# Kernel tuning notes

Hardware: AMD Instinct MI355X
Metric: run time of the kernel (lower is better)

Reference implementation:

```python
import jax, jax.numpy as jnp
import numpy as np

B, S, D, H = 2, 2048, 512, 8


def setup_inputs() -> dict:
    key = jax.random.key(0)
    ks = jax.random.split(key, 9)
    scale = 1.0 / np.sqrt(D)
    x = jax.random.normal(ks[0], (B, S, D), dtype=jnp.float32)
    # Per-head full-width projections, stacked over heads: [H, D, D]
    Wq = jax.random.normal(ks[1], (H, D, D), dtype=jnp.float32) * scale
    Wk = jax.random.normal(ks[2], (H, D, D), dtype=jnp.float32) * scale
    Wv = jax.random.normal(ks[3], (H, D, D), dtype=jnp.float32) * scale
    bq = jax.random.normal(ks[4], (H, D), dtype=jnp.float32) * 0.01
    bk = jax.random.normal(ks[5], (H, D), dtype=jnp.float32) * 0.01
    bv = jax.random.normal(ks[6], (H, D), dtype=jnp.float32) * 0.01
    Wo = jax.random.normal(ks[7], (H * D, D), dtype=jnp.float32) * (1.0 / np.sqrt(H * D))
    bo = jax.random.normal(ks[8], (D,), dtype=jnp.float32) * 0.01
    return {"x": x, "Wq": Wq, "bq": bq, "Wk": Wk, "bk": bk, "Wv": Wv, "bv": bv, "Wo": Wo, "bo": bo}


def reference(x, Wq, bq, Wk, bk, Wv, bv, Wo, bo):
    # Batched per-head projections: [B,S,D] x [H,D,E] -> [B,H,S,E]
    q = jnp.einsum('bsd,hde->bhse', x, Wq) + bq[None, :, None, :]
    k = jnp.einsum('bsd,hde->bhse', x, Wk) + bk[None, :, None, :]
    v = jnp.einsum('bsd,hde->bhse', x, Wv) + bv[None, :, None, :]
    # NOTE: original module has NO 1/sqrt(d) scaling
    scores = jnp.einsum('bhse,bhte->bhst', q, k)  # [B,H,S,S]
    attn = jax.nn.softmax(scores, axis=-1)
    out = jnp.einsum('bhst,bhte->bhse', attn, v)  # [B,H,S,D]
    # Concat heads along feature dim: [B,S,H*D]
    cat = out.transpose(0, 2, 1, 3).reshape(B, S, H * D)
    return cat @ Wo + bo
```

## Files before the change

### kernel.cpp

```cpp
#include <hip/hip_runtime.h>

typedef _Float16 f16;
typedef _Float16 f16x8 __attribute__((ext_vector_type(8)));
typedef float f32x4 __attribute__((ext_vector_type(4)));

#define B_ 2
#define S_ 2048
#define D_ 512
#define H_ 8

__device__ inline void async_ld16(const void* g, void* l) {
  __builtin_amdgcn_global_load_lds((__attribute__((address_space(1))) void*)(g),
                                   (__attribute__((address_space(3))) void*)(l),
                                   16, 0, 0);
}

__global__ __launch_bounds__(256) void cvt_f16(const float* __restrict__ src,
                                               f16* __restrict__ dst, long n) {
  long i = (long)blockIdx.x * 256 + threadIdx.x;
  if (i >= n) return;
  dst[i] = (f16)src[i];
}

__global__ __launch_bounds__(256) void transpose_f32(const float* __restrict__ src,
                                                     f16* __restrict__ dst, int R, int C) {
  __shared__ float t[32][33];
  size_t zoff = (size_t)blockIdx.z * R * C;
  const float* s = src + zoff;
  int tx = threadIdx.x;
  int ty = threadIdx.y;
  int c0 = blockIdx.x * 32, r0 = blockIdx.y * 32;
#pragma unroll
  for (int i = 0; i < 4; ++i)
    t[ty + i * 8][tx] = s[(size_t)(r0 + ty + i * 8) * C + c0 + tx];
  __syncthreads();
#pragma unroll
  for (int i = 0; i < 4; ++i)
    dst[zoff + (size_t)(c0 + ty + i * 8) * R + r0 + tx] = (f16)t[tx][ty + i * 8];
}

__global__ __launch_bounds__(256) void reduce_out(const float* __restrict__ part,
                                                  const float* __restrict__ bo,
                                                  float* __restrict__ out, long n, int nslab) {
  long i = (long)blockIdx.x * 256 + threadIdx.x;
  if (i >= n) return;
  float v = bo[i & (D_ - 1)];
  for (int s = 0; s < nslab; ++s) v += part[(long)s * n + i];
  out[i] = v;
}

struct GemmArgs {
  const f16 *A, *Bm;
  void* C;
  const float* bias;
  float* Mloc;
  int K, lda, ldb, ldc;
  int zbase, NG, PBG;
  long sAp, sAb, sAg, sAz;
  long sBp, sBb, sBg, sBz;
  long sCp, sCb, sCg, sCz;
  long sbp, sbb, sbg, sbz;
  long sMlz;
};

template <typename OutT, int BIAS, bool PEXP>
__global__ __launch_bounds__(256) void gemm_nt(GemmArgs p) {
  int zloc = blockIdx.z;
  int zi = p.zbase + zloc;
  int pp = zi / p.PBG; int rz = zi - pp * p.PBG;
  int bb = rz / p.NG;  int g = rz - bb * p.NG;
  const f16* A  = p.A + (pp * p.sAp + bb * p.sAb + g * p.sAg + (long)zloc * p.sAz);
  const f16* Bm = p.Bm + (pp * p.sBp + bb * p.sBb + g * p.sBg + (long)zloc * p.sBz);
  OutT* C = (OutT*)p.C + (pp * p.sCp + bb * p.sCb + g * p.sCg + (long)zloc * p.sCz);
  const float* bias = nullptr;
  if (BIAS) bias = p.bias + (pp * p.sbp + bb * p.sbb + g * p.sbg + (long)zloc * p.sbz);

  __shared__ f16 lA[4096];
  __shared__ f16 lB[4096];
  __shared__ float lMx[PEXP ? 256 : 1];

  int tid = threadIdx.x;
  int lane = tid & 63;
  int w = tid >> 6;
  int wm = (w >> 1) << 6;
  int wn = (w & 1) << 6;
  long bm = (long)blockIdx.y * 128;
  long bn = (long)blockIdx.x * 128;

  f32x4 acc[4][4] = {};
  int qd = lane >> 4;
  int fr = lane & 15;

  int q0 = tid, q1 = tid + 256;
  int r0s = q0 >> 2, c0s = (q0 & 3) ^ ((r0s >> 1) & 3);
  int r1s = q1 >> 2, c1s = (q1 & 3) ^ ((r1s >> 1) & 3);

  for (int k0 = 0; k0 < p.K; k0 += 32) {
    long oa0 = (bm + r0s) * (long)p.lda + (k0 + c0s * 8);
    long oa1 = (bm + r1s) * (long)p.lda + (k0 + c1s * 8);
    long ob0 = (bn + r0s) * (long)p.ldb + (k0 + c0s * 8);
    long ob1 = (bn + r1s) * (long)p.ldb + (k0 + c1s * 8);
    __syncthreads();
    async_ld16(A + oa0,  lA + (size_t)q0 * 8);
    async_ld16(A + oa1,  lA + (size_t)q1 * 8);
    async_ld16(Bm + ob0, lB + (size_t)q0 * 8);
    async_ld16(Bm + ob1, lB + (size_t)q1 * 8);
    __syncthreads();

    f16x8 ah[4], bh[4];
#pragma unroll
    for (int i = 0; i < 4; ++i) {
      int m = wm + i * 16 + fr;
      ah[i] = *(const f16x8*)(lA + ((size_t)m * 4 + (qd ^ ((m >> 1) & 3))) * 8);
      int n = wn + i * 16 + fr;
      bh[i] = *(const f16x8*)(lB + ((size_t)n * 4 + (qd ^ ((n >> 1) & 3))) * 8);
    }
#pragma unroll
    for (int i = 0; i < 4; ++i)
#pragma unroll
      for (int j = 0; j < 4; ++j)
        acc[i][j] = __builtin_amdgcn_mfma_f32_16x16x32_f16(ah[i], bh[j], acc[i][j], 0, 0, 0);
  }

  int rr0 = qd * 4;
  if (PEXP) {
#pragma unroll
    for (int i = 0; i < 4; ++i) {
#pragma unroll
      for (int r = 0; r < 4; ++r) {
        float v = fmaxf(fmaxf(acc[i][0][r], acc[i][1][r]),
                        fmaxf(acc[i][2][r], acc[i][3][r]));
        v = fmaxf(v, __shfl_xor(v, 1, 64));
        v = fmaxf(v, __shfl_xor(v, 2, 64));
        v = fmaxf(v, __shfl_xor(v, 4, 64));
        v = fmaxf(v, __shfl_xor(v, 8, 64));
        if (fr == 0) lMx[(w & 1) * 128 + wm + i * 16 + rr0 + r] = v;
      }
    }
    __syncthreads();
    if (tid < 128) {
      float ml = fmaxf(lMx[tid], lMx[128 + tid]);
      p.Mloc[(long)zloc * p.sMlz + (long)blockIdx.x * S_ + bm + tid] = ml;
    }
#pragma unroll
    for (int i = 0; i < 4; ++i) {
#pragma unroll
      for (int r = 0; r < 4; ++r) {
        int rl = wm + i * 16 + rr0 + r;
        float ml = fmaxf(lMx[rl], lMx[128 + rl]);
        long row = bm + rl;
#pragma unroll
        for (int j = 0; j < 4; ++j) {
          long col = bn + wn + j * 16 + fr;
          ((f16*)C)[row * (long)p.ldc + col] = (f16)__expf(acc[i][j][r] - ml);
        }
      }
    }
  } else {
#pragma unroll
    for (int i = 0; i < 4; ++i) {
#pragma unroll
      for (int j = 0; j < 4; ++j) {
#pragma unroll
        for (int r = 0; r < 4; ++r) {
          long row = bm + wm + i * 16 + rr0 + r;
          long col = bn + wn + j * 16 + fr;
          float v = acc[i][j][r];
          if (BIAS == 1) v += bias[col];
          if (BIAS == 2) v += bias[row];
          C[row * (long)p.ldc + col] = (OutT)v;
        }
      }
    }
  }
}

struct QkvArgs {
  const f16 *xh, *wqk, *wv;
  f16 *qk, *vT;
  const float *bqk, *bv;
};
__global__ __launch_bounds__(256) void qkv_proj(QkvArgs p) {
  const long SD = (long)S_ * D_, DD = (long)D_ * D_, DS = (long)D_ * S_;
  int zi = blockIdx.z;
  int pp = zi >> 4;
  int r = zi & 15;
  int b = r >> 3, h = r & 7;
  int bid = blockIdx.x;
  const f16 *A, *Bm;
  f16* C;
  const float* bias;
  long bm, bn;
  int ldc;
  bool biasRow;
  if (pp < 2) {
    A = p.xh + (long)b * SD;
    Bm = p.wqk + ((long)pp * 8 + h) * DD;
    C = p.qk + (long)zi * SD;
    bias = p.bqk + ((long)pp * 8 + h) * D_;
    bm = (long)(bid >> 2) * 128; bn = (long)(bid & 3) * 128;
    ldc = D_; biasRow = false;
  } else {
    A = p.wv + (long)h * DD;
    Bm = p.xh + (long)b * SD;
    C = p.vT + (long)(b * 8 + h) * DS;
    bias = p.bv + (long)h * D_;
    bm = (long)(bid >> 4) * 128; bn = (long)(bid & 15) * 128;
    ldc = S_; biasRow = true;
  }

  __shared__ f16 lA[4096];
  __shared__ f16 lB[4096];

  int tid = threadIdx.x;
  int lane = tid & 63;
  int w = tid >> 6;
  int wm = (w >> 1) << 6;
  int wn = (w & 1) << 6;

  f32x4 acc[4][4] = {};
  int qd = lane >> 4;
  int fr = lane & 15;

  int q0 = tid, q1 = tid + 256;
  int r0s = q0 >> 2, c0s = (q0 & 3) ^ ((r0s >> 1) & 3);
  int r1s = q1 >> 2, c1s = (q1 & 3) ^ ((r1s >> 1) & 3);

  for (int k0 = 0; k0 < D_; k0 += 32) {
    long oa0 = (bm + r0s) * (long)D_ + (k0 + c0s * 8);
    long oa1 = (bm + r1s) * (long)D_ + (k0 + c1s * 8);
    long ob0 = (bn + r0s) * (long)D_ + (k0 + c0s * 8);
    long ob1 = (bn + r1s) * (long)D_ + (k0 + c1s * 8);
    __syncthreads();
    async_ld16(A + oa0,  lA + (size_t)q0 * 8);
    async_ld16(A + oa1,  lA + (size_t)q1 * 8);
    async_ld16(Bm + ob0, lB + (size_t)q0 * 8);
    async_ld16(Bm + ob1, lB + (size_t)q1 * 8);
    __syncthreads();

    f16x8 ah[4], bh[4];
#pragma unroll
    for (int i = 0; i < 4; ++i) {
      int m = wm + i * 16 + fr;
      ah[i] = *(const f16x8*)(lA + ((size_t)m * 4 + (qd ^ ((m >> 1) & 3))) * 8);
      int n = wn + i * 16 + fr;
      bh[i] = *(const f16x8*)(lB + ((size_t)n * 4 + (qd ^ ((n >> 1) & 3))) * 8);
    }
#pragma unroll
    for (int i = 0; i < 4; ++i)
#pragma unroll
      for (int j = 0; j < 4; ++j)
        acc[i][j] = __builtin_amdgcn_mfma_f32_16x16x32_f16(ah[i], bh[j], acc[i][j], 0, 0, 0);
  }

  int rr0 = qd * 4;
#pragma unroll
  for (int i = 0; i < 4; ++i) {
#pragma unroll
    for (int j = 0; j < 4; ++j) {
#pragma unroll
      for (int r = 0; r < 4; ++r) {
        long row = bm + wm + i * 16 + rr0 + r;
        long col = bn + wn + j * 16 + fr;
        float v = acc[i][j][r] + (biasRow ? bias[row] : bias[col]);
        C[row * (long)ldc + col] = (f16)v;
      }
    }
  }
}

struct PvArgs {
  const f16* S; const float* Ml; const f16* V; f16* C;
  int ldc, zbase, NG;
  long sVz, sCb, sCg;
};
__global__ __launch_bounds__(256) void pv_flash(PvArgs p) {
  int zloc = blockIdx.z;
  int zi = p.zbase + zloc;
  int bb = zi / p.NG; int g = zi - bb * p.NG;
  const f16* Sm = p.S + (long)zloc * S_ * S_;
  const float* Ml = p.Ml + (long)zloc * 16 * S_;
  const f16* V = p.V + (long)zloc * p.sVz;
  f16* C = p.C + bb * p.sCb + g * p.sCg;

  __shared__ f16 lP[2][64 * 32];
  __shared__ f16 lV[2][128 * 32];

  int tid = threadIdx.x;
  int lane = tid & 63;
  int w = tid >> 6;
  long bm = (long)blockIdx.y * 64;
  long bn = (long)blockIdx.x * 128;
  int e0 = (w & 1) << 6;
  int m0 = (w >> 1) << 5;

  int qd = lane >> 4;
  int fr = lane & 15;

  f32x4 acc[2][4] = {};
  f32x4 lacc[2] = {};
  f16x8 ones;
#pragma unroll
  for (int j = 0; j < 8; ++j) ones[j] = (f16)1.0f;

  float mg[2];
#pragma unroll
  for (int i = 0; i < 2; ++i) {
    float m = -1e30f;
#pragma unroll
    for (int cb = 0; cb < 16; ++cb)
      m = fmaxf(m, Ml[cb * S_ + bm + m0 + i * 16 + fr]);
    mg[i] = m;
  }
  f16 al16[2];

  int rs = tid >> 2, cs = (tid & 3) ^ ((rs >> 1) & 3);

  for (int k0 = 0; k0 < S_; k0 += 64) {
    if ((k0 & 127) == 0) {
      int cb = k0 >> 7;
#pragma unroll
      for (int i = 0; i < 2; ++i)
        al16[i] = (f16)__expf(Ml[cb * S_ + bm + m0 + i * 16 + fr] - mg[i]);
    }
    __syncthreads();
#pragma unroll
    for (int t = 0; t < 2; ++t) {
      async_ld16(Sm + (bm + rs) * (long)S_ + (k0 + t * 32 + cs * 8),
                 lP[t] + (size_t)tid * 8);
#pragma unroll
      for (int j = 0; j < 2; ++j) {
        int q = j * 256 + tid;
        int rv = q >> 2, cv = (q & 3) ^ ((rv >> 1) & 3);
        async_ld16(V + (bn + rv) * (long)S_ + (k0 + t * 32 + cv * 8),
                   lV[t] + (size_t)q * 8);
      }
    }
    __syncthreads();

#pragma unroll
    for (int t = 0; t < 2; ++t) {
      f16x8 ah[2], bh[4];
#pragma unroll
      for (int i = 0; i < 2; ++i) {
        int m = m0 + i * 16 + fr;
        ah[i] = *(const f16x8*)(lP[t] + ((size_t)m * 4 + (qd ^ ((m >> 1) & 3))) * 8);
#pragma unroll
        for (int j = 0; j < 8; ++j) ah[i][j] *= al16[i];
      }
#pragma unroll
      for (int j = 0; j < 4; ++j) {
        int n = e0 + j * 16 + fr;
        bh[j] = *(const f16x8*)(lV[t] + ((size_t)n * 4 + (qd ^ ((n >> 1) & 3))) * 8);
      }
#pragma unroll
      for (int i = 0; i < 2; ++i) {
        lacc[i] = __builtin_amdgcn_mfma_f32_16x16x32_f16(ah[i], ones, lacc[i], 0, 0, 0);
#pragma unroll
        for (int j = 0; j < 4; ++j)
          acc[i][j] = __builtin_amdgcn_mfma_f32_16x16x32_f16(ah[i], bh[j], acc[i][j], 0, 0, 0);
      }
    }
  }

  int rr0 = qd * 4;
#pragma unroll
  for (int i = 0; i < 2; ++i) {
    float inv[4];
#pragma unroll
    for (int r = 0; r < 4; ++r) inv[r] = 1.0f / lacc[i][r];
#pragma unroll
    for (int j = 0; j < 4; ++j) {
#pragma unroll
      for (int r = 0; r < 4; ++r) {
        long row = bm + m0 + i * 16 + rr0 + r;
        long col = bn + e0 + j * 16 + fr;
        C[row * (long)p.ldc + col] = (f16)(acc[i][j][r] * inv[r]);
      }
    }
  }
}

extern "C" void kernel_launch(void* const* d_in, const int* in_sizes, int n_in,
                              void* d_out, int out_size, void* d_ws, size_t ws_size,
                              hipStream_t stream) {
  const float* x  = (const float*)d_in[0];
  const float* Wq = (const float*)d_in[1];
  const float* bq = (const float*)d_in[2];
  const float* Wk = (const float*)d_in[3];
  const float* bk = (const float*)d_in[4];
  const float* Wv = (const float*)d_in[5];
  const float* bv = (const float*)d_in[6];
  const float* Wo = (const float*)d_in[7];
  const float* bo = (const float*)d_in[8];
  float* out = (float*)d_out;

  auto al = [](size_t v) { return (v + 255) & ~(size_t)255; };
  const size_t eX = (size_t)B_ * S_ * D_;
  const size_t eW = (size_t)H_ * D_ * D_;
  const size_t eSS = (size_t)S_ * S_;
  const long SD = (long)S_ * D_;
  const long DD = (long)D_ * D_;
  const long DS = (long)D_ * S_;

  size_t fixed = al(eX * 2) + al(2 * eW * 2) + al(eW * 2) + al(eW * 2)
               + al(2ULL * H_ * D_ * 4);
  int NB = 1, GH = 1, GS = 1; bool found = false;
  for (int nb = 2; nb >= 1 && !found; --nb)
    for (int gh = 8; gh >= 1 && !found; gh >>= 1)
      for (int gs = nb * gh; gs >= 1 && !found; gs >>= 1) {
        size_t need = fixed + al((size_t)nb * S_ * H_ * D_ * 2)
                    + al(2ULL * nb * gh * S_ * D_ * 2)
                    + al((size_t)nb * gh * D_ * S_ * 2)
                    + al(4ULL * nb * SD * 4)
                    + al((size_t)gs * eSS * 2)
                    + al((size_t)gs * 16 * S_ * 4);
        if (need <= ws_size) { NB = nb; GH = gh; GS = gs; found = true; }
      }

  char* p0 = (char*)d_ws;
  size_t off = 0;
  f16* xh    = (f16*)(p0 + off); off += al(eX * 2);
  f16* wqk   = (f16*)(p0 + off); off += al(2 * eW * 2);
  f16* wv    = (f16*)(p0 + off); off += al(eW * 2);
  f16* wo    = (f16*)(p0 + off); off += al(eW * 2);
  float* bqk = (float*)(p0 + off); off += al(2ULL * H_ * D_ * 4);
  f16* catb  = (f16*)(p0 + off); off += al((size_t)NB * S_ * H_ * D_ * 2);
  f16* qk    = (f16*)(p0 + off); off += al(2ULL * NB * GH * S_ * D_ * 2);
  f16* vT    = (f16*)(p0 + off); off += al((size_t)NB * GH * D_ * S_ * 2);
  float* opart = (float*)(p0 + off); off += al(4ULL * NB * SD * 4);
  f16* scores = (f16*)(p0 + off); off += al((size_t)GS * eSS * 2);
  float* mloc = (float*)(p0 + off);

  cvt_f16<<<dim3((unsigned)((eX + 255) / 256)), 256, 0, stream>>>(x, xh, (long)eX);
  dim3 tb(32, 8, 1);
  transpose_f32<<<dim3(16, 16, H_), tb, 0, stream>>>(Wq, wqk, D_, D_);
  transpose_f32<<<dim3(16, 16, H_), tb, 0, stream>>>(Wk, wqk + eW, D_, D_);
  transpose_f32<<<dim3(16, 16, H_), tb, 0, stream>>>(Wv, wv, D_, D_);
  transpose_f32<<<dim3(16, 128, 1), tb, 0, stream>>>(Wo, wo, H_ * D_, D_);
  hipMemcpyAsync(bqk, bq, (size_t)H_ * D_ * 4, hipMemcpyDeviceToDevice, stream);
  hipMemcpyAsync(bqk + H_ * D_, bk, (size_t)H_ * D_ * 4, hipMemcpyDeviceToDevice, stream);

  for (int b0 = 0; b0 < B_; b0 += NB) {
    for (int h0 = 0; h0 < H_; h0 += GH) {
      if (NB == 2 && GH == 8) {
        QkvArgs a{xh, wqk, wv, qk, vT, bqk, bv};
        qkv_proj<<<dim3(64, 1, 48), 256, 0, stream>>>(a);
      } else {
        {
          GemmArgs a{};
          a.A = xh + (long)b0 * SD;
          a.Bm = wqk + (long)h0 * DD;
          a.C = qk; a.bias = bqk + (long)h0 * D_;
          a.K = D_; a.lda = D_; a.ldb = D_; a.ldc = D_;
          a.zbase = 0; a.NG = GH; a.PBG = NB * GH;
          a.sAb = SD;
          a.sBp = (long)H_ * DD; a.sBg = DD;
          a.sCz = SD;
          a.sbp = (long)H_ * D_; a.sbg = D_;
          gemm_nt<f16, 1, false><<<dim3(4, 16, 2 * NB * GH), 256, 0, stream>>>(a);
        }
        {
          GemmArgs a{};
          a.A = wv + (long)h0 * DD; a.Bm = xh + (long)b0 * SD;
          a.C = vT; a.bias = bv + (long)h0 * D_;
          a.K = D_; a.lda = D_; a.ldb = D_; a.ldc = S_;
          a.zbase = 0; a.NG = GH; a.PBG = NB * GH;
          a.sAg = DD;
          a.sBb = SD;
          a.sCz = DS;
          a.sbg = D_;
          gemm_nt<f16, 2, false><<<dim3(16, 4, NB * GH), 256, 0, stream>>>(a);
        }
      }
      for (int g0 = 0; g0 < NB * GH; g0 += GS) {
        {
          GemmArgs a{};
          a.A = qk + (long)g0 * SD;
          a.Bm = qk + ((long)NB * GH + g0) * SD;
          a.C = scores; a.Mloc = mloc;
          a.K = D_; a.lda = D_; a.ldb = D_; a.ldc = S_;
          a.zbase = g0; a.NG = GH; a.PBG = NB * GH;
          a.sAz = SD; a.sBz = SD; a.sCz = (long)eSS;
          a.sMlz = 16L * S_;
          gemm_nt<f16, 0, true><<<dim3(16, 16, GS), 256, 0, stream>>>(a);
        }
        {
          PvArgs a{};
          a.S = scores; a.Ml = mloc; a.V = vT + (long)g0 * DS;
          a.C = catb + (long)h0 * D_;
          a.ldc = H_ * D_; a.zbase = g0; a.NG = GH;
          a.sVz = DS; a.sCb = (long)S_ * H_ * D_; a.sCg = D_;
          pv_flash<<<dim3(4, S_ / 64, GS), 256, 0, stream>>>(a);
        }
      }
    }
    {
      GemmArgs a{};
      a.A = catb; a.Bm = wo;
      a.C = opart;
      a.K = 1024; a.lda = H_ * D_; a.ldb = H_ * D_; a.ldc = D_;
      a.zbase = 0; a.NG = 4; a.PBG = NB * 4;
      a.sAb = (long)S_ * H_ * D_; a.sAg = 1024;
      a.sBg = 1024;
      a.sCb = SD; a.sCg = (long)NB * SD;
      gemm_nt<float, 0, false><<<dim3(4, 16, NB * 4), 256, 0, stream>>>(a);
    }
    reduce_out<<<dim3((unsigned)(((long)NB * SD + 255) / 256)), 256, 0, stream>>>(
        opart, bo, out + (long)b0 * SD, (long)NB * SD, 4);
  }
}
```

Measured before the change: 471.6 us.

## Rewrite QKV projection as 256x256 tile, 8-wave, double-buffered pipelined GEMM

```diff
diff --git a/kernel.cpp b/kernel.cpp
--- a/kernel.cpp
+++ b/kernel.cpp
@@ -180,7 +180,52 @@
   f16 *qk, *vT;
   const float *bqk, *bv;
 };
-__global__ __launch_bounds__(256) void qkv_proj(QkvArgs p) {
+
+template <int MH, int NH>
+__device__ inline void phase_mfma(const f16* L, int cur, int qr, int qc,
+                                  int qd, int fr, f32x4 (&acc)[2][2][4][2]) {
+  const f16* Ab = L + cur * 32768 + MH * 8192;
+  const f16* Bb = L + cur * 32768 + 16384 + NH * 8192;
+  f16x8 af[4][2], bf[2][2];
+#pragma unroll
+  for (int i = 0; i < 4; ++i) {
+    int rr = qr * 64 + i * 16 + fr;
+#pragma unroll
+    for (int ks = 0; ks < 2; ++ks) {
+      int cc = ks * 4 + qd;
+      af[i][ks] = *(const f16x8*)(Ab + ((size_t)rr * 8 + (cc ^ ((rr >> 1) & 7))) * 8);
+    }
+  }
+#pragma unroll
+  for (int j = 0; j < 2; ++j) {
+    int rr = qc * 32 + j * 16 + fr;
+#pragma unroll
+    for (int ks = 0; ks < 2; ++ks) {
+      int cc = ks * 4 + qd;
+      bf[j][ks] = *(const f16x8*)(Bb + ((size_t)rr * 8 + (cc ^ ((rr >> 1) & 7))) * 8);
+    }
+  }
+  __builtin_amdgcn_s_setprio(1);
+#pragma unroll
+  for (int i = 0; i < 4; ++i)
+#pragma unroll
+    for (int j = 0; j < 2; ++j)
+#pragma unroll
+      for (int ks = 0; ks < 2; ++ks)
+        acc[MH][NH][i][j] = __builtin_amdgcn_mfma_f32_16x16x32_f16(
+            af[i][ks], bf[j][ks], acc[MH][NH][i][j], 0, 0, 0);
+  __builtin_amdgcn_s_setprio(0);
+}
+
+#define QWAIT(N)                                              \
+  asm volatile("s_waitcnt vmcnt(" #N ")" ::: "memory");       \
+  __builtin_amdgcn_s_barrier();                               \
+  __builtin_amdgcn_sched_barrier(0);
+#define QBAR()                                                \
+  __builtin_amdgcn_s_barrier();                               \
+  __builtin_amdgcn_sched_barrier(0);
+
+__global__ __launch_bounds__(512, 2) void qkv_proj8(QkvArgs p) {
   const long SD = (long)S_ * D_, DD = (long)D_ * D_, DS = (long)D_ * S_;
   int zi = blockIdx.z;
   int pp = zi >> 4;
@@ -198,75 +243,90 @@
     Bm = p.wqk + ((long)pp * 8 + h) * DD;
     C = p.qk + (long)zi * SD;
     bias = p.bqk + ((long)pp * 8 + h) * D_;
-    bm = (long)(bid >> 2) * 128; bn = (long)(bid & 3) * 128;
+    bm = (long)(bid >> 1) * 256; bn = (long)(bid & 1) * 256;
     ldc = D_; biasRow = false;
   } else {
     A = p.wv + (long)h * DD;
     Bm = p.xh + (long)b * SD;
     C = p.vT + (long)(b * 8 + h) * DS;
     bias = p.bv + (long)h * D_;
-    bm = (long)(bid >> 4) * 128; bn = (long)(bid & 15) * 128;
+    bm = (long)(bid >> 3) * 256; bn = (long)(bid & 7) * 256;
     ldc = S_; biasRow = true;
   }
 
-  __shared__ f16 lA[4096];
-  __shared__ f16 lB[4096];
+  __shared__ f16 L[65536];
 
   int tid = threadIdx.x;
   int lane = tid & 63;
   int w = tid >> 6;
-  int wm = (w >> 1) << 6;
-  int wn = (w & 1) << 6;
-
-  f32x4 acc[4][4] = {};
-  int qd = lane >> 4;
-  int fr = lane & 15;
-
-  int q0 = tid, q1 = tid + 256;
-  int r0s = q0 >> 2, c0s = (q0 & 3) ^ ((r0s >> 1) & 3);
-  int r1s = q1 >> 2, c1s = (q1 & 3) ^ ((r1s >> 1) & 3);
-
-  for (int k0 = 0; k0 < D_; k0 += 32) {
-    long oa0 = (bm + r0s) * (long)D_ + (k0 + c0s * 8);
-    long oa1 = (bm + r1s) * (long)D_ + (k0 + c1s * 8);
-    long ob0 = (bn + r0s) * (long)D_ + (k0 + c0s * 8);
-    long ob1 = (bn + r1s) * (long)D_ + (k0 + c1s * 8);
-    __syncthreads();
-    async_ld16(A + oa0,  lA + (size_t)q0 * 8);
-    async_ld16(A + oa1,  lA + (size_t)q1 * 8);
-    async_ld16(Bm + ob0, lB + (size_t)q0 * 8);
-    async_ld16(Bm + ob1, lB + (size_t)q1 * 8);
-    __syncthreads();
-
-    f16x8 ah[4], bh[4];
-#pragma unroll
-    for (int i = 0; i < 4; ++i) {
-      int m = wm + i * 16 + fr;
-      ah[i] = *(const f16x8*)(lA + ((size_t)m * 4 + (qd ^ ((m >> 1) & 3))) * 8);
-      int n = wn + i * 16 + fr;
-      bh[i] = *(const f16x8*)(lB + ((size_t)n * 4 + (qd ^ ((n >> 1) & 3))) * 8);
-    }
-#pragma unroll
-    for (int i = 0; i < 4; ++i)
-#pragma unroll
-      for (int j = 0; j < 4; ++j)
-        acc[i][j] = __builtin_amdgcn_mfma_f32_16x16x32_f16(ah[i], bh[j], acc[i][j], 0, 0, 0);
-  }
+  int qr = w >> 2, qc = w & 3;
+  int qd = lane >> 4, fr = lane & 15;
+
+  f32x4 acc[2][2][4][2] = {};
+
+  int srl = w * 16 + (lane >> 3);
+  int sslot = lane & 7;
+
+  auto stage = [&](const f16* src, long row0, int kb, int ldsBase) {
+#pragma unroll
+    for (int k = 0; k < 2; ++k) {
+      int rl = srl + k * 8;
+      int c = sslot ^ ((rl >> 1) & 7);
+      async_ld16(src + (row0 + rl) * (long)D_ + (kb + c * 8),
+                 L + ldsBase + (w * 2 + k) * 512 + lane * 8);
+    }
+  };
+  auto iA = [&](int buf, int hh, int t) {
+    stage(A, bm + hh * 128, t * 64, buf * 32768 + hh * 8192);
+  };
+  auto iB = [&](int buf, int hh, int t) {
+    stage(Bm, bn + hh * 128, t * 64, buf * 32768 + 16384 + hh * 8192);
+  };
+
+  iA(0, 0, 0); iB(0, 0, 0); iB(0, 1, 0); iA(0, 1, 0);
+
+  int cur = 0;
+  for (int t = 0; t < 7; ++t) {
+    int nxt = cur ^ 1;
+    iA(nxt, 0, t + 1);
+    QWAIT(6)
+    phase_mfma<0, 0>(L, cur, qr, qc, qd, fr, acc);
+    iB(nxt, 0, t + 1);
+    QWAIT(6)
+    phase_mfma<0, 1>(L, cur, qr, qc, qd, fr, acc);
+    iB(nxt, 1, t + 1);
+    QWAIT(6)
+    phase_mfma<1, 0>(L, cur, qr, qc, qd, fr, acc);
+    iA(nxt, 1, t + 1);
+    QBAR()
+    phase_mfma<1, 1>(L, cur, qr, qc, qd, fr, acc);
+    cur = nxt;
+  }
+  QWAIT(4)
+  phase_mfma<0, 0>(L, cur, qr, qc, qd, fr, acc);
+  QWAIT(2)
+  phase_mfma<0, 1>(L, cur, qr, qc, qd, fr, acc);
+  QWAIT(0)
+  phase_mfma<1, 0>(L, cur, qr, qc, qd, fr, acc);
+  QBAR()
+  phase_mfma<1, 1>(L, cur, qr, qc, qd, fr, acc);
 
   int rr0 = qd * 4;
 #pragma unroll
-  for (int i = 0; i < 4; ++i) {
-#pragma unroll
-    for (int j = 0; j < 4; ++j) {
-#pragma unroll
-      for (int r = 0; r < 4; ++r) {
-        long row = bm + wm + i * 16 + rr0 + r;
-        long col = bn + wn + j * 16 + fr;
-        float v = acc[i][j][r] + (biasRow ? bias[row] : bias[col]);
-        C[row * (long)ldc + col] = (f16)v;
-      }
-    }
-  }
+  for (int mh = 0; mh < 2; ++mh)
+#pragma unroll
+    for (int nh = 0; nh < 2; ++nh)
+#pragma unroll
+      for (int i = 0; i < 4; ++i)
+#pragma unroll
+        for (int j = 0; j < 2; ++j)
+#pragma unroll
+          for (int rl = 0; rl < 4; ++rl) {
+            long row = bm + mh * 128 + qr * 64 + i * 16 + rr0 + rl;
+            long col = bn + nh * 128 + qc * 32 + j * 16 + fr;
+            float v = acc[mh][nh][i][j][rl] + (biasRow ? bias[row] : bias[col]);
+            C[row * (long)ldc + col] = (f16)v;
+          }
 }
 
 struct PvArgs {
@@ -445,7 +505,7 @@
     for (int h0 = 0; h0 < H_; h0 += GH) {
       if (NB == 2 && GH == 8) {
         QkvArgs a{xh, wqk, wv, qk, vT, bqk, bv};
-        qkv_proj<<<dim3(64, 1, 48), 256, 0, stream>>>(a);
+        qkv_proj8<<<dim3(16, 1, 48), 512, 0, stream>>>(a);
       } else {
         {
           GemmArgs a{};
```

New measurement: 488.5 us. 1.04x slower.
